# Optimization experiments

Hardware: AMD Instinct MI355X
Metric: run time of the kernel (lower is better)

## Reference

```python
import jax, jax.numpy as jnp
import numpy as np

N = 100000      # nodes
R = 8           # relations
E_DIM = 128     # embedding dim
N_EDGES = 1600000  # n * avg_degree(16)


def setup_inputs() -> dict:
    key = jax.random.key(0)
    k1, k2, k3, k4, k5 = jax.random.split(key, 5)
    x = jax.random.normal(k1, (N, E_DIM), dtype=jnp.float32)
    # xavier-ish scale for (r, e, e) relation weights
    weights = jax.random.normal(k2, (R, E_DIM, E_DIM), dtype=jnp.float32) * (1.0 / np.sqrt(E_DIM))
    edge_rel = jax.random.randint(k3, (N_EDGES,), 0, R, dtype=jnp.int32)
    edge_src = jax.random.randint(k4, (N_EDGES,), 0, N, dtype=jnp.int32)
    edge_dst = jax.random.randint(k5, (N_EDGES,), 0, N, dtype=jnp.int32)
    return dict(x=x, weights=weights, edge_rel=edge_rel, edge_src=edge_src, edge_dst=edge_dst)


def reference(x, weights, edge_rel, edge_src, edge_dst):
    n, e = x.shape
    r = weights.shape[0]
    # sparse adjacency row index: relation-block row = rel * n + dst  (shape rn)
    rows = edge_rel.astype(jnp.int32) * n + edge_dst.astype(jnp.int32)
    # row-normalized values: vals = 1 / row_degree (util.sum_sparse)
    deg = jax.ops.segment_sum(jnp.ones(rows.shape, dtype=x.dtype), rows, num_segments=r * n)
    vals = 1.0 / deg[rows]  # only evaluated at rows with >=1 edge
    # SpMM: h = graph @ x, viewed as (r, n, e)
    msgs = vals[:, None] * x[edge_src]                       # (E, e) gather
    h = jax.ops.segment_sum(msgs, rows, num_segments=r * n)  # (r*n, e) scatter-add
    h = h.reshape(r, n, e)
    # per-relation transform: (r, e_out, e_in) x (r, n, e_in) -> (n, r, e_out)
    h = jnp.einsum('rih,rnh->nri', weights, h)
    # SumUnify: relu(sum over relations)
    return jax.nn.relu(h.sum(axis=1))
```

## Files before the change

kernel.cpp:

```cpp
#include <hip/hip_runtime.h>
#include <hip/hip_bf16.h>

#define ED 128
#define RR 8
#define KTOT (RR * ED)
#define LDB 136

typedef __attribute__((ext_vector_type(8))) short short8;
typedef __attribute__((ext_vector_type(4))) float f32x4;
typedef __attribute__((ext_vector_type(4))) unsigned short u16x4;

#define RL(v, i) __builtin_amdgcn_readlane(v, i)

__device__ __forceinline__ unsigned short f2bf(float f){
  unsigned int u = __builtin_bit_cast(unsigned int, f);
  return (unsigned short)((u + 0x7fffu + ((u >> 16) & 1u)) >> 16);
}
__device__ __forceinline__ float bf2f(unsigned int lo){
  return __builtin_bit_cast(float, lo << 16);
}
__device__ __forceinline__ unsigned int packbf(float hi, float lo){
  return ((unsigned int)f2bf(hi) << 16) | f2bf(lo);
}

__global__ void cast_bf16_vec(const float* __restrict__ in, unsigned short* __restrict__ out, int n4){
  int stride = gridDim.x * blockDim.x;
  for (int i = blockIdx.x * blockDim.x + threadIdx.x; i < n4; i += stride){
    f32x4 v = __builtin_nontemporal_load((const f32x4*)(in + (size_t)i * 4));
    u16x4 o;
    o[0] = f2bf(v[0]); o[1] = f2bf(v[1]); o[2] = f2bf(v[2]); o[3] = f2bf(v[3]);
    *(u16x4*)(out + (size_t)i * 4) = o;
  }
}

__global__ void hist_rank(const int* __restrict__ rel, const int* __restrict__ dst,
                          int* __restrict__ rowcnt, int* __restrict__ rank, int E){
  int stride = gridDim.x * blockDim.x;
  for (int i = blockIdx.x * blockDim.x + threadIdx.x; i < E; i += stride)
    rank[i] = atomicAdd(&rowcnt[(dst[i] << 3) | rel[i]], 1);
}

__launch_bounds__(1024)
__global__ void scan_block_sum(const int* __restrict__ rowcnt, int* __restrict__ bsum, int m){
  __shared__ int lds[16];
  int t = threadIdx.x;
  int idx = blockIdx.x * 1024 + t;
  int v = (idx < m) ? rowcnt[idx] : 0;
#pragma unroll
  for (int o = 32; o > 0; o >>= 1) v += __shfl_down(v, o);
  if ((t & 63) == 0) lds[t >> 6] = v;
  __syncthreads();
  if (t == 0){
    int s = 0;
#pragma unroll
    for (int w = 0; w < 16; ++w) s += lds[w];
    bsum[blockIdx.x] = s;
  }
}

__launch_bounds__(1024)
__global__ void scan_bsum_par(const int* __restrict__ bsum, int* __restrict__ bscan,
                              int nb, int* __restrict__ total_out){
  __shared__ int wsum[16];
  int t = threadIdx.x, lane = t & 63, wid = t >> 6;
  int v = (t < nb) ? bsum[t] : 0;
  int incl = v;
#pragma unroll
  for (int o = 1; o < 64; o <<= 1){
    int u = __shfl_up(incl, o);
    if (lane >= o) incl += u;
  }
  if (lane == 63) wsum[wid] = incl;
  __syncthreads();
  int woff = 0;
  for (int w0 = 0; w0 < wid; ++w0) woff += wsum[w0];
  if (t < nb) bscan[t] = woff + incl - v;
  if (t == nb - 1) *total_out = woff + incl;
}

__launch_bounds__(1024)
__global__ void scan_final(const int* __restrict__ rowcnt, const int* __restrict__ bscan,
                           int* __restrict__ row_ptr, int m){
  __shared__ int wsum[16];
  int t = threadIdx.x, lane = t & 63, wid = t >> 6;
  int idx = blockIdx.x * 1024 + t;
  int v = (idx < m) ? rowcnt[idx] : 0;
  int incl = v;
#pragma unroll
  for (int o = 1; o < 64; o <<= 1){
    int u = __shfl_up(incl, o);
    if (lane >= o) incl += u;
  }
  if (lane == 63) wsum[wid] = incl;
  __syncthreads();
  int woff = bscan[blockIdx.x];
  for (int w0 = 0; w0 < wid; ++w0) woff += wsum[w0];
  if (idx < m) row_ptr[idx] = woff + incl - v;
}

__global__ void scatter_pos(const int* __restrict__ rel, const int* __restrict__ src,
                            const int* __restrict__ dst, const int* __restrict__ rank,
                            const int* __restrict__ row_ptr, int* __restrict__ payload, int E){
  int stride = gridDim.x * blockDim.x;
  for (int i = blockIdx.x * blockDim.x + threadIdx.x; i < E; i += stride){
    int key = (dst[i] << 3) | rel[i];
    payload[row_ptr[key] + rank[i]] = src[i];
  }
}

__launch_bounds__(256)
__global__ void row_agg(const unsigned short* __restrict__ xb,
                        const int* __restrict__ row_ptr8,
                        const int* __restrict__ payload,
                        unsigned short* __restrict__ h2, int n){
  int d    = (blockIdx.x * 256 + threadIdx.x) >> 6;
  int lane = threadIdx.x & 63;
  if (d >= n) return;

  int p9 = 0;
  if (lane < 9) p9 = row_ptr8[(d << 3) + lane];
  int b0  = RL(p9, 0);
  int o1  = RL(p9, 1) - b0;
  int o2  = RL(p9, 2) - b0;
  int o3  = RL(p9, 3) - b0;
  int o4  = RL(p9, 4) - b0;
  int o5  = RL(p9, 5) - b0;
  int o6  = RL(p9, 6) - b0;
  int o7  = RL(p9, 7) - b0;
  int cnt = RL(p9, 8) - b0;

  float ax0=0.f,ay0=0.f,ax1=0.f,ay1=0.f,ax2=0.f,ay2=0.f,ax3=0.f,ay3=0.f;
  float ax4=0.f,ay4=0.f,ax5=0.f,ay5=0.f,ax6=0.f,ay6=0.f,ax7=0.f,ay7=0.f;

#define ROUTE(VV, IDX) { \
    float lo = bf2f((VV) & 0xffffu), hi = bf2f((VV) >> 16); \
    if ((IDX) < o4){ \
      if ((IDX) < o2){ if ((IDX) < o1){ ax0+=lo; ay0+=hi; } else { ax1+=lo; ay1+=hi; } } \
      else           { if ((IDX) < o3){ ax2+=lo; ay2+=hi; } else { ax3+=lo; ay3+=hi; } } \
    } else { \
      if ((IDX) < o6){ if ((IDX) < o5){ ax4+=lo; ay4+=hi; } else { ax5+=lo; ay5+=hi; } } \
      else           { if ((IDX) < o7){ ax6+=lo; ay6+=hi; } else { ax7+=lo; ay7+=hi; } } \
    } }

  if (cnt <= 64){
    int pl = payload[b0 + lane];
    int e = 0;
    for (; e + 8 <= cnt; e += 8){
      int s0 = RL(pl, e);
      int s1 = RL(pl, e + 1);
      int s2 = RL(pl, e + 2);
      int s3 = RL(pl, e + 3);
      int s4 = RL(pl, e + 4);
      int s5 = RL(pl, e + 5);
      int s6 = RL(pl, e + 6);
      int s7 = RL(pl, e + 7);
      unsigned int v0 = ((const unsigned int*)(xb + ((size_t)s0 << 7)))[lane];
      unsigned int v1 = ((const unsigned int*)(xb + ((size_t)s1 << 7)))[lane];
      unsigned int v2 = ((const unsigned int*)(xb + ((size_t)s2 << 7)))[lane];
      unsigned int v3 = ((const unsigned int*)(xb + ((size_t)s3 << 7)))[lane];
      unsigned int v4 = ((const unsigned int*)(xb + ((size_t)s4 << 7)))[lane];
      unsigned int v5 = ((const unsigned int*)(xb + ((size_t)s5 << 7)))[lane];
      unsigned int v6 = ((const unsigned int*)(xb + ((size_t)s6 << 7)))[lane];
      unsigned int v7 = ((const unsigned int*)(xb + ((size_t)s7 << 7)))[lane];
      ROUTE(v0, e)
      ROUTE(v1, e + 1)
      ROUTE(v2, e + 2)
      ROUTE(v3, e + 3)
      ROUTE(v4, e + 4)
      ROUTE(v5, e + 5)
      ROUTE(v6, e + 6)
      ROUTE(v7, e + 7)
    }
    for (; e < cnt; ++e){
      int s = RL(pl, e);
      unsigned int v = ((const unsigned int*)(xb + ((size_t)s << 7)))[lane];
      ROUTE(v, e)
    }
  } else {
    for (int e = 0; e < cnt; ++e){
      int s = __builtin_amdgcn_readfirstlane(payload[b0 + e]);
      unsigned int v = ((const unsigned int*)(xb + ((size_t)s << 7)))[lane];
      ROUTE(v, e)
    }
  }
#undef ROUTE

  int c0 = o1, c1 = o2 - o1, c2 = o3 - o2, c3 = o4 - o3;
  int c4 = o5 - o4, c5 = o6 - o5, c6 = o7 - o6, c7 = cnt - o7;
  unsigned int* hp = (unsigned int*)h2 + ((size_t)d << 9) + lane;
  float sc;
  sc = c0 ? 1.f / (float)c0 : 0.f; __builtin_nontemporal_store(packbf(ay0*sc, ax0*sc), hp);
  sc = c1 ? 1.f / (float)c1 : 0.f; __builtin_nontemporal_store(packbf(ay1*sc, ax1*sc), hp + 64);
  sc = c2 ? 1.f / (float)c2 : 0.f; __builtin_nontemporal_store(packbf(ay2*sc, ax2*sc), hp + 128);
  sc = c3 ? 1.f / (float)c3 : 0.f; __builtin_nontemporal_store(packbf(ay3*sc, ax3*sc), hp + 192);
  sc = c4 ? 1.f / (float)c4 : 0.f; __builtin_nontemporal_store(packbf(ay4*sc, ax4*sc), hp + 256);
  sc = c5 ? 1.f / (float)c5 : 0.f; __builtin_nontemporal_store(packbf(ay5*sc, ax5*sc), hp + 320);
  sc = c6 ? 1.f / (float)c6 : 0.f; __builtin_nontemporal_store(packbf(ay6*sc, ax6*sc), hp + 384);
  sc = c7 ? 1.f / (float)c7 : 0.f; __builtin_nontemporal_store(packbf(ay7*sc, ax7*sc), hp + 448);
}

__launch_bounds__(256)
__global__ void gemm_out(const unsigned short* __restrict__ h2,
                         const unsigned short* __restrict__ wbb,
                         float* __restrict__ out, int n){
  __shared__ __align__(16) unsigned short lds_a[128 * LDB];
  __shared__ __align__(16) unsigned short lds_b[128 * LDB];
  const int t = threadIdx.x;
  const int wave = t >> 6, lane = t & 63;
  const int wr = wave >> 1, wc = wave & 1;
  const int dbase = blockIdx.x * 128;
  const int frow = lane & 15, kb = lane >> 4;

  f32x4 acc[4][4];
#pragma unroll
  for (int rt = 0; rt < 4; ++rt)
#pragma unroll
    for (int jt = 0; jt < 4; ++jt)
      acc[rt][jt] = (f32x4){0.f, 0.f, 0.f, 0.f};

  short8 pa[8], pb[8];
#pragma unroll
  for (int p = 0; p < 8; ++p){
    int q = p * 256 + t;
    int row = q >> 4, col = q & 15;
    int gr = dbase + row; if (gr >= n) gr = n - 1;
    pa[p] = __builtin_nontemporal_load((const short8*)(h2 + (size_t)gr * KTOT + col * 8));
    pb[p] = *(const short8*)(wbb + row * ED + col * 8);
  }

  for (int r = 0; r < RR; ++r){
    __syncthreads();
#pragma unroll
    for (int p = 0; p < 8; ++p){
      int q = p * 256 + t;
      int row = q >> 4, col = q & 15;
      *(short8*)&lds_a[row * LDB + col * 8] = pa[p];
      *(short8*)&lds_b[row * LDB + col * 8] = pb[p];
    }
    __syncthreads();

    if (r + 1 < RR){
#pragma unroll
      for (int p = 0; p < 8; ++p){
        int q = p * 256 + t;
        int row = q >> 4, col = q & 15;
        int gr = dbase + row; if (gr >= n) gr = n - 1;
        pa[p] = __builtin_nontemporal_load(
            (const short8*)(h2 + (size_t)gr * KTOT + (r + 1) * ED + col * 8));
        pb[p] = *(const short8*)(wbb + (size_t)(r + 1) * ED * ED + row * ED + col * 8);
      }
    }

    short8 a[4][4], b[4][4];
#pragma unroll
    for (int rt = 0; rt < 4; ++rt)
#pragma unroll
      for (int ks = 0; ks < 4; ++ks)
        a[rt][ks] = *(const short8*)&lds_a[(wr * 64 + rt * 16 + frow) * LDB + ks * 32 + kb * 8];
#pragma unroll
    for (int jt = 0; jt < 4; ++jt)
#pragma unroll
      for (int ks = 0; ks < 4; ++ks)
        b[jt][ks] = *(const short8*)&lds_b[(wc * 64 + jt * 16 + frow) * LDB + ks * 32 + kb * 8];
#pragma unroll
    for (int rt = 0; rt < 4; ++rt)
#pragma unroll
      for (int jt = 0; jt < 4; ++jt)
#pragma unroll
        for (int ks = 0; ks < 4; ++ks)
          acc[rt][jt] = __builtin_amdgcn_mfma_f32_16x16x32_bf16(a[rt][ks], b[jt][ks], acc[rt][jt], 0, 0, 0);
  }

  const int drow = (lane >> 4) * 4;
  const int dcol = lane & 15;
#pragma unroll
  for (int rt = 0; rt < 4; ++rt)
#pragma unroll
    for (int jt = 0; jt < 4; ++jt)
#pragma unroll
      for (int reg = 0; reg < 4; ++reg){
        int i = dbase + wr * 64 + rt * 16 + drow + reg;
        if (i < n)
          __builtin_nontemporal_store(fmaxf(acc[rt][jt][reg], 0.f),
                                      &out[(size_t)i * ED + wc * 64 + jt * 16 + dcol]);
      }
}

extern "C" void kernel_launch(void* const* d_in, const int* in_sizes, int n_in,
                              void* d_out, int out_size, void* d_ws, size_t ws_size,
                              hipStream_t stream){
  const float* x  = (const float*)d_in[0];
  const float* w  = (const float*)d_in[1];
  const int* erel = (const int*)d_in[2];
  const int* esrc = (const int*)d_in[3];
  const int* edst = (const int*)d_in[4];
  float* out = (float*)d_out;

  const int n = in_sizes[0] / ED;
  const int E = in_sizes[2];
  const int m = n * RR;
  const int NB = (m + 1023) / 1024;

  char* ws = (char*)d_ws;
  size_t off = 0;
  auto alloc = [&](size_t bytes) -> char* {
    char* p = ws + off;
    off += (bytes + 255) & ~(size_t)255;
    return p;
  };
  unsigned short* h2      = (unsigned short*)alloc((size_t)n * KTOT * 2);
  unsigned short* xb      = (unsigned short*)alloc((size_t)n * ED * 2);
  unsigned short* wbb     = (unsigned short*)alloc((size_t)RR * ED * ED * 2);
  int*            payload = (int*)alloc((size_t)E * 4);
  int*            row_ptr = (int*)alloc((size_t)(m + 1) * 4);
  int*            rowcnt  = (int*)alloc((size_t)m * 4);
  int*            rank    = (int*)alloc((size_t)E * 4);
  int*            bsum    = (int*)alloc((size_t)NB * 4);
  int*            bscan   = (int*)alloc((size_t)NB * 4);
  if (off > ws_size || NB > 1024) return;

  (void)hipMemsetAsync(rowcnt, 0, (size_t)m * 4, stream);

  cast_bf16_vec<<<2048, 256, 0, stream>>>(x, xb, n * ED / 4);
  cast_bf16_vec<<<128, 256, 0, stream>>>(w, wbb, RR * ED * ED / 4);
  hist_rank    <<<2048, 256, 0, stream>>>(erel, edst, rowcnt, rank, E);
  scan_block_sum<<<NB, 1024, 0, stream>>>(rowcnt, bsum, m);
  scan_bsum_par<<<1, 1024, 0, stream>>>(bsum, bscan, NB, row_ptr + m);
  scan_final   <<<NB, 1024, 0, stream>>>(rowcnt, bscan, row_ptr, m);
  scatter_pos  <<<2048, 256, 0, stream>>>(erel, esrc, edst, rank, row_ptr, payload, E);
  row_agg      <<<(n + 3) / 4, 256, 0, stream>>>(xb, row_ptr, payload, h2, n);
  gemm_out     <<<(n + 127) / 128, 256, 0, stream>>>(h2, wbb, out, n);
}
```

Baseline: 284.4 us.

## Split aggregation and GEMM into two node chunks so intermediate stays cache-resident

Runs row_agg and gemm_out in two node chunks of about 50K nodes, reusing a chunk-sized bf16 intermediate buffer and switching from nontemporal to normal stores and loads. The aim is for the roughly 100MB per-chunk intermediate to stay in the large last-level cache between the producer and consumer instead of going through HBM. This adds extra kernel launches and tail effects per chunk. It also hardcodes a chunk size, so correctness depends on n being at most twice CH.

```diff
diff --git a/kernel.cpp b/kernel.cpp
--- a/kernel.cpp
+++ b/kernel.cpp
@@ -5,6 +5,7 @@
 #define RR 8
 #define KTOT (RR * ED)
 #define LDB 136
+#define CH 50048
 
 typedef __attribute__((ext_vector_type(8))) short short8;
 typedef __attribute__((ext_vector_type(4))) float f32x4;
@@ -112,10 +113,10 @@
 __global__ void row_agg(const unsigned short* __restrict__ xb,
                         const int* __restrict__ row_ptr8,
                         const int* __restrict__ payload,
-                        unsigned short* __restrict__ h2, int n){
-  int d    = (blockIdx.x * 256 + threadIdx.x) >> 6;
+                        unsigned short* __restrict__ h2buf, int d0, int d1){
+  int d    = d0 + ((blockIdx.x * 256 + threadIdx.x) >> 6);
   int lane = threadIdx.x & 63;
-  if (d >= n) return;
+  if (d >= d1) return;
 
   int p9 = 0;
   if (lane < 9) p9 = row_ptr8[(d << 3) + lane];
@@ -187,28 +188,28 @@
 
   int c0 = o1, c1 = o2 - o1, c2 = o3 - o2, c3 = o4 - o3;
   int c4 = o5 - o4, c5 = o6 - o5, c6 = o7 - o6, c7 = cnt - o7;
-  unsigned int* hp = (unsigned int*)h2 + ((size_t)d << 9) + lane;
+  unsigned int* hp = (unsigned int*)h2buf + ((size_t)(d - d0) << 9) + lane;
   float sc;
-  sc = c0 ? 1.f / (float)c0 : 0.f; __builtin_nontemporal_store(packbf(ay0*sc, ax0*sc), hp);
-  sc = c1 ? 1.f / (float)c1 : 0.f; __builtin_nontemporal_store(packbf(ay1*sc, ax1*sc), hp + 64);
-  sc = c2 ? 1.f / (float)c2 : 0.f; __builtin_nontemporal_store(packbf(ay2*sc, ax2*sc), hp + 128);
-  sc = c3 ? 1.f / (float)c3 : 0.f; __builtin_nontemporal_store(packbf(ay3*sc, ax3*sc), hp + 192);
-  sc = c4 ? 1.f / (float)c4 : 0.f; __builtin_nontemporal_store(packbf(ay4*sc, ax4*sc), hp + 256);
-  sc = c5 ? 1.f / (float)c5 : 0.f; __builtin_nontemporal_store(packbf(ay5*sc, ax5*sc), hp + 320);
-  sc = c6 ? 1.f / (float)c6 : 0.f; __builtin_nontemporal_store(packbf(ay6*sc, ax6*sc), hp + 384);
-  sc = c7 ? 1.f / (float)c7 : 0.f; __builtin_nontemporal_store(packbf(ay7*sc, ax7*sc), hp + 448);
+  sc = c0 ? 1.f / (float)c0 : 0.f; hp[0]   = packbf(ay0*sc, ax0*sc);
+  sc = c1 ? 1.f / (float)c1 : 0.f; hp[64]  = packbf(ay1*sc, ax1*sc);
+  sc = c2 ? 1.f / (float)c2 : 0.f; hp[128] = packbf(ay2*sc, ax2*sc);
+  sc = c3 ? 1.f / (float)c3 : 0.f; hp[192] = packbf(ay3*sc, ax3*sc);
+  sc = c4 ? 1.f / (float)c4 : 0.f; hp[256] = packbf(ay4*sc, ax4*sc);
+  sc = c5 ? 1.f / (float)c5 : 0.f; hp[320] = packbf(ay5*sc, ax5*sc);
+  sc = c6 ? 1.f / (float)c6 : 0.f; hp[384] = packbf(ay6*sc, ax6*sc);
+  sc = c7 ? 1.f / (float)c7 : 0.f; hp[448] = packbf(ay7*sc, ax7*sc);
 }
 
 __launch_bounds__(256)
-__global__ void gemm_out(const unsigned short* __restrict__ h2,
+__global__ void gemm_out(const unsigned short* __restrict__ h2buf,
                          const unsigned short* __restrict__ wbb,
-                         float* __restrict__ out, int n){
+                         float* __restrict__ out, int d0, int d1){
   __shared__ __align__(16) unsigned short lds_a[128 * LDB];
   __shared__ __align__(16) unsigned short lds_b[128 * LDB];
   const int t = threadIdx.x;
   const int wave = t >> 6, lane = t & 63;
   const int wr = wave >> 1, wc = wave & 1;
-  const int dbase = blockIdx.x * 128;
+  const int dbase = d0 + blockIdx.x * 128;
   const int frow = lane & 15, kb = lane >> 4;
 
   f32x4 acc[4][4];
@@ -223,8 +224,8 @@
   for (int p = 0; p < 8; ++p){
     int q = p * 256 + t;
     int row = q >> 4, col = q & 15;
-    int gr = dbase + row; if (gr >= n) gr = n - 1;
-    pa[p] = __builtin_nontemporal_load((const short8*)(h2 + (size_t)gr * KTOT + col * 8));
+    int gr = dbase + row; if (gr >= d1) gr = d1 - 1;
+    pa[p] = *(const short8*)(h2buf + (size_t)(gr - d0) * KTOT + col * 8);
     pb[p] = *(const short8*)(wbb + row * ED + col * 8);
   }
 
@@ -244,9 +245,8 @@
       for (int p = 0; p < 8; ++p){
         int q = p * 256 + t;
         int row = q >> 4, col = q & 15;
-        int gr = dbase + row; if (gr >= n) gr = n - 1;
-        pa[p] = __builtin_nontemporal_load(
-            (const short8*)(h2 + (size_t)gr * KTOT + (r + 1) * ED + col * 8));
+        int gr = dbase + row; if (gr >= d1) gr = d1 - 1;
+        pa[p] = *(const short8*)(h2buf + (size_t)(gr - d0) * KTOT + (r + 1) * ED + col * 8);
         pb[p] = *(const short8*)(wbb + (size_t)(r + 1) * ED * ED + row * ED + col * 8);
       }
     }
@@ -280,7 +280,7 @@
 #pragma unroll
       for (int reg = 0; reg < 4; ++reg){
         int i = dbase + wr * 64 + rt * 16 + drow + reg;
-        if (i < n)
+        if (i < d1)
           __builtin_nontemporal_store(fmaxf(acc[rt][jt][reg], 0.f),
                                       &out[(size_t)i * ED + wc * 64 + jt * 16 + dcol]);
       }
@@ -308,7 +308,7 @@
     off += (bytes + 255) & ~(size_t)255;
     return p;
   };
-  unsigned short* h2      = (unsigned short*)alloc((size_t)n * KTOT * 2);
+  unsigned short* h2buf   = (unsigned short*)alloc((size_t)CH * KTOT * 2);
   unsigned short* xb      = (unsigned short*)alloc((size_t)n * ED * 2);
   unsigned short* wbb     = (unsigned short*)alloc((size_t)RR * ED * ED * 2);
   int*            payload = (int*)alloc((size_t)E * 4);
@@ -328,6 +328,12 @@
   scan_bsum_par<<<1, 1024, 0, stream>>>(bsum, bscan, NB, row_ptr + m);
   scan_final   <<<NB, 1024, 0, stream>>>(rowcnt, bscan, row_ptr, m);
   scatter_pos  <<<2048, 256, 0, stream>>>(erel, esrc, edst, rank, row_ptr, payload, E);
-  row_agg      <<<(n + 3) / 4, 256, 0, stream>>>(xb, row_ptr, payload, h2, n);
-  gemm_out     <<<(n + 127) / 128, 256, 0, stream>>>(h2, wbb, out, n);
-}
+
+  for (int c = 0; c < 2; ++c){
+    int d0 = c * CH;
+    int d1 = (c == 0) ? CH : n;
+    int nodes = d1 - d0;
+    row_agg <<<(nodes + 3) / 4, 256, 0, stream>>>(xb, row_ptr, payload, h2buf, d0, d1);
+    gemm_out<<<(nodes + 127) / 128, 256, 0, stream>>>(h2buf, wbb, out, d0, d1);
+  }
+}
```

Result: no change. 285.8 us (+0.5%).
